# Kernel optimization log

Hardware: AMD Instinct MI355X
Metric: run time of the kernel (lower is better)

Reference implementation:

```python
import jax, jax.numpy as jnp
import numpy as np

NUM_GROUPS = 32
EPS = 1e-5
HEADS = 8
DIM_HEAD = 64


def group_norm(x, w, b):
    # x: [B, C, L]; normalize over (C/G, L) per group
    B, C, L = x.shape
    xg = x.reshape(B, NUM_GROUPS, C // NUM_GROUPS, L)
    mu = jnp.mean(xg, axis=(2, 3), keepdims=True)
    var = jnp.var(xg, axis=(2, 3), keepdims=True)
    xn = ((xg - mu) * jax.lax.rsqrt(var + EPS)).reshape(B, C, L)
    return xn * w[None, :, None] + b[None, :, None]


def setup_inputs() -> dict:
    key = jax.random.key(0)
    k1, k2, k3 = jax.random.split(key, 3)
    dim, hidden = 512, HEADS * DIM_HEAD
    B, L = 4, 2048
    x = jax.random.normal(k1, (B, dim, L), dtype=jnp.float32)
    gn_w = jnp.ones((dim,), jnp.float32)
    gn_b = jnp.zeros((dim,), jnp.float32)
    w_qkv = jax.random.normal(k2, (3 * hidden, dim), jnp.float32) * (dim ** -0.5)
    w_out = jax.random.normal(k3, (dim, hidden), jnp.float32) * (hidden ** -0.5)
    b_out = jnp.zeros((dim,), jnp.float32)
    return {"x": x, "gn_w": gn_w, "gn_b": gn_b, "w_qkv": w_qkv, "w_out": w_out, "b_out": b_out}


def reference(x, gn_w, gn_b, w_qkv, w_out, b_out):
    B, C, L = x.shape
    scale = DIM_HEAD ** -0.5
    nx = group_norm(x, gn_w, gn_b)
    # 1x1 conv == channel matmul: [3H*D, C] x [B, C, L] -> [B, 3H*D, L]
    qkv = jnp.einsum('oc,bcl->bol', w_qkv, nx)
    q, k, v = jnp.split(qkv, 3, axis=1)
    rs = lambda t: t.reshape(B, HEADS, DIM_HEAD, L)
    q, k, v = rs(q) * scale, rs(k), rs(v)
    sim = jnp.einsum('bhdi,bhdj->bhij', q, k)         # [B,H,L,L]
    attn = jax.nn.softmax(sim, axis=-1)
    out = jnp.einsum('bhij,bhdj->bhdi', attn, v)       # [B,H,D,L]
    out = out.reshape(B, HEADS * DIM_HEAD, L)
    proj = jnp.einsum('oc,bcl->bol', w_out, out) + b_out[None, :, None]
    return proj + x
```

## Files before the change

kernel.cpp:

```cpp
#include <hip/hip_runtime.h>

#define DEVI __device__ __forceinline__

typedef unsigned short u16;
typedef unsigned int u32;
typedef __attribute__((ext_vector_type(8))) __bf16 bf16x8;
typedef __attribute__((ext_vector_type(4))) __bf16 bf16x4;
typedef __attribute__((ext_vector_type(4))) float f32x4;

DEVI u16 f2bf(float f){
  u32 u = __float_as_uint(f);
  return (u16)((u + 0x7FFFu + ((u >> 16) & 1u)) >> 16);
}

__global__ __launch_bounds__(256) void gnstat_kernel(const float* __restrict__ x,
                                                     float2* __restrict__ pstat){
  int bg = blockIdx.x >> 2, qt = blockIdx.x & 3;
  const float4* xin = (const float4*)(x + (size_t)bg*32768 + qt*8192);
  int tid = threadIdx.x;
  float s1 = 0.f, s2 = 0.f;
  #pragma unroll
  for (int i = 0; i < 8; ++i){
    float4 v = xin[tid + i*256];
    s1 += v.x + v.y + v.z + v.w;
    s2 += v.x*v.x + v.y*v.y + v.z*v.z + v.w*v.w;
  }
  __shared__ float red[8];
  int lane = tid & 63, w = tid >> 6;
  for (int off = 32; off; off >>= 1){
    s1 += __shfl_down(s1, off);
    s2 += __shfl_down(s2, off);
  }
  if (lane == 0){ red[w] = s1; red[4 + w] = s2; }
  __syncthreads();
  if (tid == 0){
    pstat[blockIdx.x] = make_float2(red[0]+red[1]+red[2]+red[3],
                                    red[4]+red[5]+red[6]+red[7]);
  }
}

__global__ __launch_bounds__(128) void gnfin_kernel(const float2* __restrict__ pstat,
                                                    float2* __restrict__ stat){
  int t = threadIdx.x;
  float s1 = 0.f, s2 = 0.f;
  #pragma unroll
  for (int i = 0; i < 4; ++i){
    float2 p = pstat[t*4 + i];
    s1 += p.x; s2 += p.y;
  }
  float mu = s1 * (1.f/32768.f);
  float var = s2 * (1.f/32768.f) - mu*mu;
  stat[t] = make_float2(mu, rsqrtf(var + 1e-5f));
}

__global__ __launch_bounds__(256) void normtrans_kernel(const float* __restrict__ x,
                                                        const float2* __restrict__ stat,
                                                        const float* __restrict__ gw,
                                                        const float* __restrict__ gb,
                                                        u16* __restrict__ nxT){
  int b = blockIdx.z, c0 = blockIdx.y * 64, l0 = blockIdx.x * 64;
  __shared__ u16 T[64][72];
  int tid = threadIdx.x;
  #pragma unroll
  for (int rep = 0; rep < 2; ++rep){
    int task = tid + rep*256;
    int r = task >> 3, cc = task & 7;
    int ch = c0 + r;
    float2 st = stat[b*32 + (ch >> 4)];
    float ga = gw[ch] * st.y;
    float be = gb[ch] - st.x * ga;
    const float4* src = (const float4*)(x + ((size_t)(b*512 + ch))*2048 + l0 + cc*8);
    float4 v0 = src[0], v1 = src[1];
    ushort4 o0, o1;
    o0.x = f2bf(v0.x*ga + be); o0.y = f2bf(v0.y*ga + be);
    o0.z = f2bf(v0.z*ga + be); o0.w = f2bf(v0.w*ga + be);
    o1.x = f2bf(v1.x*ga + be); o1.y = f2bf(v1.y*ga + be);
    o1.z = f2bf(v1.z*ga + be); o1.w = f2bf(v1.w*ga + be);
    *(ushort4*)&T[r][cc*8]     = o0;
    *(ushort4*)&T[r][cc*8 + 4] = o1;
  }
  __syncthreads();
  #pragma unroll
  for (int rep = 0; rep < 2; ++rep){
    int task = tid + rep*256;
    int r = task >> 3, cc = task & 7;
    u16 tmp[8];
    #pragma unroll
    for (int i = 0; i < 8; ++i) tmp[i] = T[cc*8 + i][r];
    *(uint4*)(nxT + ((size_t)(b*2048 + l0 + r))*512 + c0 + cc*8) = *(uint4*)tmp;
  }
}

__global__ __launch_bounds__(256) void castw_kernel(const float* __restrict__ wq,
                                                    const float* __restrict__ wo,
                                                    u16* __restrict__ wqb,
                                                    u16* __restrict__ wob){
  int t = blockIdx.x * 256 + threadIdx.x;
  const int NQ4 = (1536*512)/4;
  float4 v; u16* dst;
  if (t < NQ4){ v = ((const float4*)wq)[t]; dst = wqb + t*4; }
  else        { int u_ = t - NQ4; v = ((const float4*)wo)[u_]; dst = wob + u_*4; }
  ushort4 s;
  s.x = f2bf(v.x); s.y = f2bf(v.y); s.z = f2bf(v.z); s.w = f2bf(v.w);
  *(ushort4*)dst = s;
}

template<int MODE>
__global__ __launch_bounds__(256) void gemm_kernel(const u16* __restrict__ A,
                                                   const u16* __restrict__ Bm,
                                                   u16* __restrict__ q_o,
                                                   u16* __restrict__ k_o,
                                                   u16* __restrict__ v_o,
                                                   const float* __restrict__ bo,
                                                   const float* __restrict__ xres,
                                                   float* __restrict__ out){
  int b  = blockIdx.z;
  int n0 = blockIdx.x * 128, m0 = blockIdx.y * 128;
  int tid = threadIdx.x, w = tid >> 6, lane = tid & 63, lq = lane >> 4, lr = lane & 15;
  int wm = (w >> 1) * 64, wn = (w & 1) * 64;
  __shared__ u16 Al[128][40], Bl[128][40];
  f32x4 acc[4][4] = {};
  const u16* Bb = Bm + (size_t)b * 2048 * 512;

  for (int k0 = 0; k0 < 512; k0 += 32){
    #pragma unroll
    for (int rep = 0; rep < 2; ++rep){
      int task = tid + rep*256;
      int row = task >> 2, kc = task & 3;
      *(uint4*)&Al[row][kc*8] = *(const uint4*)(A  + (size_t)(m0+row)*512 + k0 + kc*8);
      *(uint4*)&Bl[row][kc*8] = *(const uint4*)(Bb + (size_t)(n0+row)*512 + k0 + kc*8);
    }
    __syncthreads();
    bf16x8 af[4], bfr[4];
    #pragma unroll
    for (int i = 0; i < 4; ++i) af[i]  = *(const bf16x8*)&Al[wm + i*16 + lr][lq*8];
    #pragma unroll
    for (int j = 0; j < 4; ++j) bfr[j] = *(const bf16x8*)&Bl[wn + j*16 + lr][lq*8];
    #pragma unroll
    for (int i = 0; i < 4; ++i)
      #pragma unroll
      for (int j = 0; j < 4; ++j)
        acc[i][j] = __builtin_amdgcn_mfma_f32_16x16x32_bf16(af[i], bfr[j], acc[i][j], 0, 0, 0);
    __syncthreads();
  }

  if (MODE == 0){
    const float QSCALE = 0.125f * 1.4426950408889634f;
    #pragma unroll
    for (int i = 0; i < 4; ++i){
      int o0  = m0 + wm + i*16 + lq*4;
      int cls = o0 >> 9;
      int hh  = (o0 >> 6) & 7;
      int d0  = o0 & 63;
      #pragma unroll
      for (int j = 0; j < 4; ++j){
        int l = n0 + wn + j*16 + lr;
        f32x4 v = acc[i][j];
        if (cls == 0){
          ushort4 s;
          s.x = f2bf(v[0]*QSCALE); s.y = f2bf(v[1]*QSCALE);
          s.z = f2bf(v[2]*QSCALE); s.w = f2bf(v[3]*QSCALE);
          *(ushort4*)(q_o + (((size_t)(b*8+hh))*2048 + l)*64 + d0) = s;
        } else if (cls == 1){
          ushort4 s;
          s.x = f2bf(v[0]); s.y = f2bf(v[1]); s.z = f2bf(v[2]); s.w = f2bf(v[3]);
          *(ushort4*)(k_o + (((size_t)(b*8+hh))*2048 + l)*64 + d0) = s;
        } else {
          #pragma unroll
          for (int r = 0; r < 4; ++r)
            v_o[(((size_t)(b*8+hh))*64 + d0 + r)*2048 + l] = f2bf(v[r]);
        }
      }
    }
  } else {
    #pragma unroll
    for (int i = 0; i < 4; ++i){
      int o0 = m0 + wm + i*16 + lq*4;
      #pragma unroll
      for (int j = 0; j < 4; ++j){
        int l = n0 + wn + j*16 + lr;
        #pragma unroll
        for (int r = 0; r < 4; ++r){
          int o = o0 + r;
          size_t idx = ((size_t)b*512 + o)*2048 + l;
          out[idx] = acc[i][j][r] + bo[o] + xres[idx];
        }
      }
    }
  }
}

__global__ __launch_bounds__(256) void attn_kernel(const u16* __restrict__ qT,
                                                   const u16* __restrict__ kT,
                                                   const u16* __restrict__ vv,
                                                   u16* __restrict__ ao){
  int flat = blockIdx.x;
  int xcd = flat & 7, t = flat >> 3;
  int bh = xcd*4 + (t & 3);
  int qb = t >> 2;
  int tid = threadIdx.x, w = tid >> 6, lane = tid & 63, lq = lane >> 4, lr = lane & 15;
  int i0 = qb*64 + w*16;
  size_t headoff = (size_t)bh * 2048 * 64;
  __shared__ u16 Kl[64][72], Vl[64][72], Pl[4][16][72];

  bf16x8 qf0 = *(const bf16x8*)(qT + headoff + (size_t)(i0 + lr)*64 + lq*8);
  bf16x8 qf1 = *(const bf16x8*)(qT + headoff + (size_t)(i0 + lr)*64 + 32 + lq*8);

  f32x4 of[4] = {};
  float mrow = -1e30f, lrow = 0.f;

  for (int j0 = 0; j0 < 2048; j0 += 64){
    #pragma unroll
    for (int rep = 0; rep < 2; ++rep){
      int task = tid + rep*256;
      int r = task >> 3, cc = task & 7;
      *(uint4*)&Kl[r][cc*8] = *(const uint4*)(kT + headoff + (size_t)(j0 + r)*64 + cc*8);
      *(uint4*)&Vl[r][cc*8] = *(const uint4*)(vv + headoff + (size_t)r*2048 + j0 + cc*8);
    }
    __syncthreads();

    f32x4 sa[4] = {};
    __builtin_amdgcn_s_setprio(1);
    #pragma unroll
    for (int jt = 0; jt < 4; ++jt){
      bf16x8 kf0 = *(const bf16x8*)&Kl[jt*16 + lr][lq*8];
      bf16x8 kf1 = *(const bf16x8*)&Kl[jt*16 + lr][32 + lq*8];
      sa[jt] = __builtin_amdgcn_mfma_f32_16x16x32_bf16(kf0, qf0, sa[jt], 0, 0, 0);
      sa[jt] = __builtin_amdgcn_mfma_f32_16x16x32_bf16(kf1, qf1, sa[jt], 0, 0, 0);
    }
    __builtin_amdgcn_s_setprio(0);

    float cm = sa[0][0];
    #pragma unroll
    for (int jt = 0; jt < 4; ++jt)
      #pragma unroll
      for (int r = 0; r < 4; ++r) cm = fmaxf(cm, sa[jt][r]);
    cm = fmaxf(cm, __shfl_xor(cm, 16));
    cm = fmaxf(cm, __shfl_xor(cm, 32));
    float nm = fmaxf(mrow, cm);
    float alpha = __builtin_amdgcn_exp2f(mrow - nm);
    mrow = nm;
    float rs = 0.f;
    #pragma unroll
    for (int jt = 0; jt < 4; ++jt)
      #pragma unroll
      for (int r = 0; r < 4; ++r){
        float p = __builtin_amdgcn_exp2f(sa[jt][r] - nm);
        sa[jt][r] = p; rs += p;
      }
    rs += __shfl_xor(rs, 16);
    rs += __shfl_xor(rs, 32);
    lrow = lrow*alpha + rs;

    #pragma unroll
    for (int jt = 0; jt < 4; ++jt){
      bf16x4 pv;
      #pragma unroll
      for (int r = 0; r < 4; ++r) pv[r] = (__bf16)sa[jt][r];
      *(bf16x4*)&Pl[w][lr][jt*16 + lq*4] = pv;
    }

    float a0 = __shfl(alpha, lq*4 + 0, 16);
    float a1 = __shfl(alpha, lq*4 + 1, 16);
    float a2 = __shfl(alpha, lq*4 + 2, 16);
    float a3 = __shfl(alpha, lq*4 + 3, 16);
    #pragma unroll
    for (int dt = 0; dt < 4; ++dt){
      f32x4 o = of[dt];
      o[0] *= a0; o[1] *= a1; o[2] *= a2; o[3] *= a3;
      of[dt] = o;
    }

    __builtin_amdgcn_s_setprio(1);
    #pragma unroll
    for (int jk = 0; jk < 2; ++jk){
      bf16x8 pa = *(const bf16x8*)&Pl[w][lr][jk*32 + lq*8];
      #pragma unroll
      for (int dt = 0; dt < 4; ++dt){
        bf16x8 vb = *(const bf16x8*)&Vl[dt*16 + lr][jk*32 + lq*8];
        of[dt] = __builtin_amdgcn_mfma_f32_16x16x32_bf16(pa, vb, of[dt], 0, 0, 0);
      }
    }
    __builtin_amdgcn_s_setprio(0);
    __syncthreads();
  }

  float inv = 1.f / lrow;
  float i0v = __shfl(inv, lq*4 + 0, 16);
  float i1v = __shfl(inv, lq*4 + 1, 16);
  float i2v = __shfl(inv, lq*4 + 2, 16);
  float i3v = __shfl(inv, lq*4 + 3, 16);
  int b = bh >> 3, h = bh & 7;
  #pragma unroll
  for (int dt = 0; dt < 4; ++dt){
    size_t base = ((size_t)(b*2048) + i0 + lq*4)*512 + h*64 + dt*16 + lr;
    ao[base        ] = f2bf(of[dt][0]*i0v);
    ao[base +   512] = f2bf(of[dt][1]*i1v);
    ao[base + 2*512] = f2bf(of[dt][2]*i2v);
    ao[base + 3*512] = f2bf(of[dt][3]*i3v);
  }
}

extern "C" void kernel_launch(void* const* d_in, const int* in_sizes, int n_in,
                              void* d_out, int out_size, void* d_ws, size_t ws_size,
                              hipStream_t stream) {
  const float* x    = (const float*)d_in[0];
  const float* gw   = (const float*)d_in[1];
  const float* gb   = (const float*)d_in[2];
  const float* wqkv = (const float*)d_in[3];
  const float* wout = (const float*)d_in[4];
  const float* bout = (const float*)d_in[5];
  float* out = (float*)d_out;
  char* ws = (char*)d_ws;

  const size_t MB8 = (size_t)4*512*2048*2;
  u16* ao  = (u16*)(ws);
  u16* nxT = (u16*)(ws + MB8);
  u16* wqb = (u16*)(ws + 2*MB8);
  u16* wob = (u16*)(ws + 2*MB8 + 1572864);
  u16* qT  = (u16*)(ws + 2*MB8 + 2097152);
  u16* kT  = qT + (size_t)4*8*2048*64;
  u16* vv  = kT + (size_t)4*8*2048*64;
  float2* pstat = (float2*)qT;
  float2* stat  = (float2*)((char*)qT + 8192);

  gnstat_kernel<<<512, 256, 0, stream>>>(x, pstat);
  gnfin_kernel<<<1, 128, 0, stream>>>(pstat, stat);
  castw_kernel<<<1024, 256, 0, stream>>>(wqkv, wout, wqb, wob);
  normtrans_kernel<<<dim3(32, 8, 4), 256, 0, stream>>>(x, stat, gw, gb, nxT);
  gemm_kernel<0><<<dim3(16, 12, 4), 256, 0, stream>>>(wqb, nxT, qT, kT, vv,
                                                      nullptr, nullptr, nullptr);
  attn_kernel<<<1024, 256, 0, stream>>>(qT, kT, vv, ao);
  gemm_kernel<1><<<dim3(16, 4, 4), 256, 0, stream>>>(wob, ao, nullptr, nullptr, nullptr,
                                                     bout, x, out);
}
```

Baseline: 204.6 us.

## Rewrite attention with 32x32 MFMA, register-only P, and fragment-ordered K/V layout

The QKV GEMM epilogue now writes K and V in a pre-swizzled MFMA fragment order, so the attention kernel loads operands straight from global memory into registers with no LDS staging or block barriers. Attention switches to 32x32x16 MFMA with 32 queries per wave and 128 per block, which halves the grid. The softmax probabilities are packed to bf16 and exchanged across half-waves with shuffles instead of a round trip through LDS. Rescaling of the running max is done lazily, only when the max grows by more than a threshold. The cost is that each wave now fetches K/V from global or L2 on its own, with no reuse across the block, and the threshold rescale relies on exp2 headroom in fp32.

Result: faster. 193.7 us (-5.3%).

```diff
diff --git a/kernel.cpp b/kernel.cpp
--- a/kernel.cpp
+++ b/kernel.cpp
@@ -6,11 +6,18 @@
 typedef unsigned int u32;
 typedef __attribute__((ext_vector_type(8))) __bf16 bf16x8;
 typedef __attribute__((ext_vector_type(4))) __bf16 bf16x4;
+typedef __attribute__((ext_vector_type(2))) __bf16 bf16x2;
 typedef __attribute__((ext_vector_type(4))) float f32x4;
+typedef __attribute__((ext_vector_type(16))) float f32x16;
+typedef __attribute__((ext_vector_type(4))) u32 u32x4;
 
 DEVI u16 f2bf(float f){
   u32 u = __float_as_uint(f);
   return (u16)((u + 0x7FFFu + ((u >> 16) & 1u)) >> 16);
+}
+DEVI u32 pk2(float lo, float hi){
+  bf16x2 t; t[0] = (__bf16)lo; t[1] = (__bf16)hi;
+  return __builtin_bit_cast(u32, t);
 }
 
 __global__ __launch_bounds__(256) void gnstat_kernel(const float* __restrict__ x,
@@ -152,6 +159,7 @@
       int cls = o0 >> 9;
       int hh  = (o0 >> 6) & 7;
       int d0  = o0 & 63;
+      size_t hbase = (size_t)(b*8+hh) * 2048 * 64;
       #pragma unroll
       for (int j = 0; j < 4; ++j){
         int l = n0 + wn + j*16 + lr;
@@ -160,15 +168,19 @@
           ushort4 s;
           s.x = f2bf(v[0]*QSCALE); s.y = f2bf(v[1]*QSCALE);
           s.z = f2bf(v[2]*QSCALE); s.w = f2bf(v[3]*QSCALE);
-          *(ushort4*)(q_o + (((size_t)(b*8+hh))*2048 + l)*64 + d0) = s;
+          *(ushort4*)(q_o + hbase + (size_t)l*64 + d0) = s;
         } else if (cls == 1){
+          size_t off = (size_t)(((l>>5)*4 + (d0>>4)))*512
+                     + ((d0>>3)&1)*256 + (l&31)*8 + (d0&7);
           ushort4 s;
           s.x = f2bf(v[0]); s.y = f2bf(v[1]); s.z = f2bf(v[2]); s.w = f2bf(v[3]);
-          *(ushort4*)(k_o + (((size_t)(b*8+hh))*2048 + l)*64 + d0) = s;
+          *(ushort4*)(k_o + hbase + off) = s;
         } else {
+          size_t off = (size_t)(((l>>4)*2 + (d0>>5)))*512
+                     + ((l>>3)&1)*256 + (l&7);
           #pragma unroll
           for (int r = 0; r < 4; ++r)
-            v_o[(((size_t)(b*8+hh))*64 + d0 + r)*2048 + l] = f2bf(v[r]);
+            v_o[hbase + off + ((d0+r)&31)*8] = f2bf(v[r]);
         }
       }
     }
@@ -191,113 +203,108 @@
 }
 
 __global__ __launch_bounds__(256) void attn_kernel(const u16* __restrict__ qT,
-                                                   const u16* __restrict__ kT,
-                                                   const u16* __restrict__ vv,
+                                                   const u16* __restrict__ kF,
+                                                   const u16* __restrict__ vF,
                                                    u16* __restrict__ ao){
   int flat = blockIdx.x;
   int xcd = flat & 7, t = flat >> 3;
   int bh = xcd*4 + (t & 3);
   int qb = t >> 2;
-  int tid = threadIdx.x, w = tid >> 6, lane = tid & 63, lq = lane >> 4, lr = lane & 15;
-  int i0 = qb*64 + w*16;
-  size_t headoff = (size_t)bh * 2048 * 64;
-  __shared__ u16 Kl[64][72], Vl[64][72], Pl[4][16][72];
-
-  bf16x8 qf0 = *(const bf16x8*)(qT + headoff + (size_t)(i0 + lr)*64 + lq*8);
-  bf16x8 qf1 = *(const bf16x8*)(qT + headoff + (size_t)(i0 + lr)*64 + 32 + lq*8);
-
-  f32x4 of[4] = {};
-  float mrow = -1e30f, lrow = 0.f;
-
-  for (int j0 = 0; j0 < 2048; j0 += 64){
-    #pragma unroll
-    for (int rep = 0; rep < 2; ++rep){
-      int task = tid + rep*256;
-      int r = task >> 3, cc = task & 7;
-      *(uint4*)&Kl[r][cc*8] = *(const uint4*)(kT + headoff + (size_t)(j0 + r)*64 + cc*8);
-      *(uint4*)&Vl[r][cc*8] = *(const uint4*)(vv + headoff + (size_t)r*2048 + j0 + cc*8);
-    }
-    __syncthreads();
-
-    f32x4 sa[4] = {};
-    __builtin_amdgcn_s_setprio(1);
-    #pragma unroll
-    for (int jt = 0; jt < 4; ++jt){
-      bf16x8 kf0 = *(const bf16x8*)&Kl[jt*16 + lr][lq*8];
-      bf16x8 kf1 = *(const bf16x8*)&Kl[jt*16 + lr][32 + lq*8];
-      sa[jt] = __builtin_amdgcn_mfma_f32_16x16x32_bf16(kf0, qf0, sa[jt], 0, 0, 0);
-      sa[jt] = __builtin_amdgcn_mfma_f32_16x16x32_bf16(kf1, qf1, sa[jt], 0, 0, 0);
-    }
-    __builtin_amdgcn_s_setprio(0);
-
-    float cm = sa[0][0];
-    #pragma unroll
-    for (int jt = 0; jt < 4; ++jt)
+  int tid = threadIdx.x, w = tid >> 6, l = tid & 63;
+  int l31 = l & 31, h = l >> 5;
+  int q0 = qb*128 + w*32;
+  size_t hoff = (size_t)bh * 2048 * 64;
+
+  const u16* qp = qT + hoff + (size_t)(q0 + l31)*64 + 8*h;
+  bf16x8 qf0 = *(const bf16x8*)(qp);
+  bf16x8 qf1 = *(const bf16x8*)(qp + 16);
+  bf16x8 qf2 = *(const bf16x8*)(qp + 32);
+  bf16x8 qf3 = *(const bf16x8*)(qp + 48);
+
+  const u16* kbase = kF + hoff + (size_t)l*8;
+  const u16* vbase = vF + hoff + (size_t)l*8;
+
+  f32x16 o0 = {}, o1 = {};
+  float m = -1e30f, lsum = 0.f;
+
+  for (int tile = 0; tile < 64; ++tile){
+    const u16* kt = kbase + tile*2048;
+    bf16x8 kf0 = *(const bf16x8*)(kt);
+    bf16x8 kf1 = *(const bf16x8*)(kt + 512);
+    bf16x8 kf2 = *(const bf16x8*)(kt + 1024);
+    bf16x8 kf3 = *(const bf16x8*)(kt + 1536);
+
+    f32x16 s = {};
+    s = __builtin_amdgcn_mfma_f32_32x32x16_bf16(kf0, qf0, s, 0, 0, 0);
+    s = __builtin_amdgcn_mfma_f32_32x32x16_bf16(kf1, qf1, s, 0, 0, 0);
+    s = __builtin_amdgcn_mfma_f32_32x32x16_bf16(kf2, qf2, s, 0, 0, 0);
+    s = __builtin_amdgcn_mfma_f32_32x32x16_bf16(kf3, qf3, s, 0, 0, 0);
+
+    float cm = s[0];
+    #pragma unroll
+    for (int i = 1; i < 16; ++i) cm = fmaxf(cm, s[i]);
+    cm = fmaxf(cm, __shfl_xor(cm, 32));
+
+    if (__any(cm > m + 8.f)){
+      float nm = fmaxf(m, cm);
+      float alpha = __builtin_amdgcn_exp2f(m - nm);
+      m = nm; lsum *= alpha;
       #pragma unroll
-      for (int r = 0; r < 4; ++r) cm = fmaxf(cm, sa[jt][r]);
-    cm = fmaxf(cm, __shfl_xor(cm, 16));
-    cm = fmaxf(cm, __shfl_xor(cm, 32));
-    float nm = fmaxf(mrow, cm);
-    float alpha = __builtin_amdgcn_exp2f(mrow - nm);
-    mrow = nm;
-    float rs = 0.f;
-    #pragma unroll
-    for (int jt = 0; jt < 4; ++jt)
-      #pragma unroll
-      for (int r = 0; r < 4; ++r){
-        float p = __builtin_amdgcn_exp2f(sa[jt][r] - nm);
-        sa[jt][r] = p; rs += p;
-      }
-    rs += __shfl_xor(rs, 16);
+      for (int i = 0; i < 16; ++i){ o0[i] *= alpha; o1[i] *= alpha; }
+    }
+
+    float p[16]; float rs = 0.f;
+    #pragma unroll
+    for (int i = 0; i < 16; ++i){
+      p[i] = __builtin_amdgcn_exp2f(s[i] - m);
+      rs += p[i];
+    }
     rs += __shfl_xor(rs, 32);
-    lrow = lrow*alpha + rs;
-
-    #pragma unroll
-    for (int jt = 0; jt < 4; ++jt){
-      bf16x4 pv;
-      #pragma unroll
-      for (int r = 0; r < 4; ++r) pv[r] = (__bf16)sa[jt][r];
-      *(bf16x4*)&Pl[w][lr][jt*16 + lq*4] = pv;
-    }
-
-    float a0 = __shfl(alpha, lq*4 + 0, 16);
-    float a1 = __shfl(alpha, lq*4 + 1, 16);
-    float a2 = __shfl(alpha, lq*4 + 2, 16);
-    float a3 = __shfl(alpha, lq*4 + 3, 16);
-    #pragma unroll
-    for (int dt = 0; dt < 4; ++dt){
-      f32x4 o = of[dt];
-      o[0] *= a0; o[1] *= a1; o[2] *= a2; o[3] *= a3;
-      of[dt] = o;
-    }
-
-    __builtin_amdgcn_s_setprio(1);
-    #pragma unroll
-    for (int jk = 0; jk < 2; ++jk){
-      bf16x8 pa = *(const bf16x8*)&Pl[w][lr][jk*32 + lq*8];
-      #pragma unroll
-      for (int dt = 0; dt < 4; ++dt){
-        bf16x8 vb = *(const bf16x8*)&Vl[dt*16 + lr][jk*32 + lq*8];
-        of[dt] = __builtin_amdgcn_mfma_f32_16x16x32_bf16(pa, vb, of[dt], 0, 0, 0);
-      }
-    }
-    __builtin_amdgcn_s_setprio(0);
-    __syncthreads();
-  }
-
-  float inv = 1.f / lrow;
-  float i0v = __shfl(inv, lq*4 + 0, 16);
-  float i1v = __shfl(inv, lq*4 + 1, 16);
-  float i2v = __shfl(inv, lq*4 + 2, 16);
-  float i3v = __shfl(inv, lq*4 + 3, 16);
-  int b = bh >> 3, h = bh & 7;
-  #pragma unroll
-  for (int dt = 0; dt < 4; ++dt){
-    size_t base = ((size_t)(b*2048) + i0 + lq*4)*512 + h*64 + dt*16 + lr;
-    ao[base        ] = f2bf(of[dt][0]*i0v);
-    ao[base +   512] = f2bf(of[dt][1]*i1v);
-    ao[base + 2*512] = f2bf(of[dt][2]*i2v);
-    ao[base + 3*512] = f2bf(of[dt][3]*i3v);
+    lsum += rs;
+
+    u32 a0 = pk2(p[0],  p[1]),  a1 = pk2(p[2],  p[3]);
+    u32 a2 = pk2(p[4],  p[5]),  a3 = pk2(p[6],  p[7]);
+    u32 a4 = pk2(p[8],  p[9]),  a5 = pk2(p[10], p[11]);
+    u32 a6 = pk2(p[12], p[13]), a7 = pk2(p[14], p[15]);
+    u32 x0 = __shfl_xor((int)a0, 32), x1 = __shfl_xor((int)a1, 32);
+    u32 x2 = __shfl_xor((int)a2, 32), x3 = __shfl_xor((int)a3, 32);
+    u32 x4 = __shfl_xor((int)a4, 32), x5 = __shfl_xor((int)a5, 32);
+    u32 x6 = __shfl_xor((int)a6, 32), x7 = __shfl_xor((int)a7, 32);
+    u32x4 wb0, wb1;
+    wb0[0] = h ? x2 : a0;  wb0[1] = h ? x3 : a1;
+    wb0[2] = h ? a2 : x0;  wb0[3] = h ? a3 : x1;
+    wb1[0] = h ? x6 : a4;  wb1[1] = h ? x7 : a5;
+    wb1[2] = h ? a6 : x4;  wb1[3] = h ? a7 : x5;
+    bf16x8 B0 = __builtin_bit_cast(bf16x8, wb0);
+    bf16x8 B1 = __builtin_bit_cast(bf16x8, wb1);
+
+    const u16* vt = vbase + tile*2048;
+    bf16x8 vf00 = *(const bf16x8*)(vt);
+    bf16x8 vf01 = *(const bf16x8*)(vt + 512);
+    bf16x8 vf10 = *(const bf16x8*)(vt + 1024);
+    bf16x8 vf11 = *(const bf16x8*)(vt + 1536);
+    o0 = __builtin_amdgcn_mfma_f32_32x32x16_bf16(vf00, B0, o0, 0, 0, 0);
+    o1 = __builtin_amdgcn_mfma_f32_32x32x16_bf16(vf01, B0, o1, 0, 0, 0);
+    o0 = __builtin_amdgcn_mfma_f32_32x32x16_bf16(vf10, B1, o0, 0, 0, 0);
+    o1 = __builtin_amdgcn_mfma_f32_32x32x16_bf16(vf11, B1, o1, 0, 0, 0);
+  }
+
+  float inv = 1.f / lsum;
+  int b_ = bh >> 3, hh = bh & 7;
+  size_t obase = ((size_t)(b_*2048) + q0 + l31)*512 + hh*64 + 4*h;
+  #pragma unroll
+  for (int s4 = 0; s4 < 4; ++s4){
+    ushort4 st;
+    st.x = f2bf(o0[s4*4+0]*inv); st.y = f2bf(o0[s4*4+1]*inv);
+    st.z = f2bf(o0[s4*4+2]*inv); st.w = f2bf(o0[s4*4+3]*inv);
+    *(ushort4*)(ao + obase + s4*8) = st;
+  }
+  #pragma unroll
+  for (int s4 = 0; s4 < 4; ++s4){
+    ushort4 st;
+    st.x = f2bf(o1[s4*4+0]*inv); st.y = f2bf(o1[s4*4+1]*inv);
+    st.z = f2bf(o1[s4*4+2]*inv); st.w = f2bf(o1[s4*4+3]*inv);
+    *(ushort4*)(ao + obase + 32 + s4*8) = st;
   }
 }
 
@@ -319,8 +326,8 @@
   u16* wqb = (u16*)(ws + 2*MB8);
   u16* wob = (u16*)(ws + 2*MB8 + 1572864);
   u16* qT  = (u16*)(ws + 2*MB8 + 2097152);
-  u16* kT  = qT + (size_t)4*8*2048*64;
-  u16* vv  = kT + (size_t)4*8*2048*64;
+  u16* kF  = qT + (size_t)4*8*2048*64;
+  u16* vF  = kF + (size_t)4*8*2048*64;
   float2* pstat = (float2*)qT;
   float2* stat  = (float2*)((char*)qT + 8192);
 
@@ -328,9 +335,9 @@
   gnfin_kernel<<<1, 128, 0, stream>>>(pstat, stat);
   castw_kernel<<<1024, 256, 0, stream>>>(wqkv, wout, wqb, wob);
   normtrans_kernel<<<dim3(32, 8, 4), 256, 0, stream>>>(x, stat, gw, gb, nxT);
-  gemm_kernel<0><<<dim3(16, 12, 4), 256, 0, stream>>>(wqb, nxT, qT, kT, vv,
+  gemm_kernel<0><<<dim3(16, 12, 4), 256, 0, stream>>>(wqb, nxT, qT, kF, vF,
                                                       nullptr, nullptr, nullptr);
-  attn_kernel<<<1024, 256, 0, stream>>>(qT, kT, vv, ao);
+  attn_kernel<<<512, 256, 0, stream>>>(qT, kF, vF, ao);
   gemm_kernel<1><<<dim3(16, 4, 4), 256, 0, stream>>>(wob, ao, nullptr, nullptr, nullptr,
                                                      bout, x, out);
 }
```
